# Kernel tuning notes

Measured on AMD Instinct MI355X. Metric: run time of the kernel, lower is better.

Reference implementation:

```python
import jax, jax.numpy as jnp
import numpy as np

B, T, I, H, C, S, V = 32, 64, 300, 168, 168, 512, 50257


def setup_inputs() -> dict:
    key = jax.random.key(0)
    ks = jax.random.split(key, 10)
    s = 0.05
    return {
        "x": jax.random.normal(ks[0], (B, T, I), jnp.float32),
        "context": jax.random.normal(ks[1], (B, S, C), jnp.float32),
        "context_lengths": jax.random.randint(ks[2], (B,), 1, S + 1),
        "W_ih": jax.random.normal(ks[3], (4 * H, I + C), jnp.float32) * s,
        "W_hh": jax.random.normal(ks[4], (4 * H, H), jnp.float32) * s,
        "b_ih": jnp.zeros((4 * H,), jnp.float32),
        "b_hh": jnp.zeros((4 * H,), jnp.float32),
        "att_Wx": jax.random.normal(ks[5], (H, H), jnp.float32) * s,
        "att_Ws": jax.random.normal(ks[6], (C, H), jnp.float32) * s,
        "att_b": jnp.zeros((H,), jnp.float32),
        "att_v": jax.random.normal(ks[7], (H,), jnp.float32) * s,
        "W_dec": jax.random.normal(ks[8], (V, H), jnp.float32) * s,
    }


def reference(x, context, context_lengths, W_ih, W_hh, b_ih, b_hh,
              att_Wx, att_Ws, att_b, att_v, W_dec):
    # x: (B, T, I); context: (B, S, C)
    b, t, _ = x.shape
    s_len = context.shape[1]
    h_dim = W_hh.shape[1]
    dtype = x.dtype

    # valid-position mask for attention over source context
    mask = jnp.arange(s_len)[None, :] < context_lengths[:, None]  # (B, S)
    # seq projection is time-invariant: precompute once outside the step loop
    seq_proj = jnp.einsum('bsc,ca->bsa', context, att_Ws)  # (B, S, H)

    h0 = jnp.zeros((b, h_dim), dtype)
    c0 = jnp.zeros((b, h_dim), dtype)

    def step(carry, x_t):
        h, c = carry
        # MLP (additive) attention: v . tanh(Wx h + Ws seq + b)
        e = jnp.einsum('bsa,a->bs',
                       jnp.tanh((h @ att_Wx)[:, None, :] + seq_proj + att_b),
                       att_v)  # (B, S)
        e = jnp.where(mask, e, jnp.asarray(-1e9, dtype))
        w = jax.nn.softmax(e, axis=-1)
        attn_ctx = jnp.einsum('bs,bsc->bc', w, context)  # (B, C)

        # concat input with attended context, single-layer LSTM cell
        rnn_in = jnp.concatenate([x_t, attn_ctx], axis=1)  # (B, I+C)
        gates = rnn_in @ W_ih.T + b_ih + h @ W_hh.T + b_hh  # (B, 4H)
        i_g, f_g, g_g, o_g = jnp.split(gates, 4, axis=1)    # torch ifgo order
        c_new = jax.nn.sigmoid(f_g) * c + jax.nn.sigmoid(i_g) * jnp.tanh(g_g)
        h_new = jax.nn.sigmoid(o_g) * jnp.tanh(c_new)

        dec = h_new @ W_dec.T  # (B, V), bias-free decode
        return (h_new, c_new), dec

    _, decs = jax.lax.scan(step, (h0, c0), jnp.swapaxes(x, 0, 1))  # (T, B, V)
    return jnp.swapaxes(decs, 0, 1)  # (B, T, V)
```

## Files before the change

kernel.cpp:

```cpp
#include <hip/hip_runtime.h>
#include <stdint.h>

#define BB 32
#define TT 64
#define ID 300
#define HH 168
#define SS 512
#define VV 50257
#define G4 672
#define IC 468
#define KP 192
#define NP 50304
#define NJ 8
#define RPB 21
#define CPB 84
#define KK 336
#define WKP 88
#define EPAD 170
#define SBLK 64

typedef float f32x4 __attribute__((ext_vector_type(4)));
typedef short bf16x8 __attribute__((ext_vector_type(8)));

__device__ __forceinline__ float bf2f(unsigned short u) {
  union { unsigned int i; float f; } v; v.i = ((unsigned int)u) << 16; return v.f;
}
__device__ __forceinline__ unsigned short f2bf(float f) {
  union { float f; unsigned int u; } v; v.f = f;
  unsigned int r = v.u + 0x7fffu + ((v.u >> 16) & 1u);
  return (unsigned short)(r >> 16);
}
__device__ __forceinline__ float rcpf(float x) { return __builtin_amdgcn_rcpf(x); }

__global__ void k_tr(const float* __restrict__ Wih, float* __restrict__ WihxT) {
  int idx = blockIdx.x * 256 + threadIdx.x;
  if (idx < ID * G4) {
    int k = idx / G4, i = idx - k * G4;
    WihxT[idx] = Wih[(size_t)i * IC + k];
  }
}

__global__ void k_seqproj(const float* __restrict__ ctx, const float* __restrict__ Ws,
                          unsigned short* __restrict__ ETs, unsigned short* __restrict__ ctxb) {
  const int b = blockIdx.x;
  const int s0 = blockIdx.y * 16;
  const int tid = threadIdx.x;
  __shared__ float ctxL[16 * HH];
  for (int idx = tid; idx < 16 * HH; idx += 256) {
    float v = ctx[(size_t)(b * SS + s0) * HH + idx];
    ctxL[idx] = v;
    ctxb[(size_t)(b * SS + s0) * HH + idx] = f2bf(v);
  }
  __syncthreads();
  #pragma unroll
  for (int o = 0; o < 11; ++o) {
    int idx = o * 256 + tid;
    if (idx < 16 * HH) {
      int s = idx / HH, h = idx - s * HH;
      const float* cr = &ctxL[s * HH];
      float acc = 0.f;
      #pragma unroll 4
      for (int c = 0; c < HH; ++c) acc = fmaf(cr[c], Ws[c * HH + h], acc);
      ETs[(size_t)(b * SS + s0 + s) * HH + h] = f2bf(__expf(2.f * acc));
    }
  }
}

__global__ void k_xproj(const float* __restrict__ x, const float* __restrict__ WihxT,
                        const float* __restrict__ bih, const float* __restrict__ bhh,
                        float* __restrict__ Xp) {
  const int t0 = blockIdx.x * 8;
  const int b = blockIdx.y;
  const int tid = threadIdx.x;
  __shared__ float xL[8 * ID];
  for (int idx = tid; idx < 8 * ID; idx += 256)
    xL[idx] = x[(size_t)(b * TT + t0) * ID + idx];
  __syncthreads();
  for (int i = tid; i < G4; i += 256) {
    float bias = bih[i] + bhh[i];
    float acc[8];
    #pragma unroll
    for (int tt = 0; tt < 8; ++tt) acc[tt] = bias;
    for (int k = 0; k < ID; ++k) {
      float w = WihxT[k * G4 + i];
      #pragma unroll
      for (int tt = 0; tt < 8; ++tt) acc[tt] += xL[tt * ID + k] * w;
    }
    #pragma unroll
    for (int tt = 0; tt < 8; ++tt)
      Xp[(size_t)(b * TT + t0 + tt) * G4 + i] = acc[tt];
  }
}

__global__ void k_wdec(const float* __restrict__ Wd, unsigned short* __restrict__ Wdb) {
  size_t idx = (size_t)blockIdx.x * 256 + threadIdx.x;
  int v = (int)(idx / KP), k = (int)(idx - (size_t)v * KP);
  float val = (v < VV && k < HH) ? Wd[(size_t)v * HH + k] : 0.f;
  Wdb[idx] = f2bf(val);
}

__global__ void k_prep(const float* __restrict__ Wih, const float* __restrict__ Whh,
                       const float* __restrict__ attWx, float* __restrict__ WgT,
                       unsigned short* __restrict__ WxS, unsigned int* __restrict__ flags,
                       unsigned short* __restrict__ hall) {
  int idx = blockIdx.x * 256 + threadIdx.x;
  const int T1 = NJ * KK * WKP;
  const int T2 = T1 + NJ * RPB * HH;
  const int T3 = T2 + 2 * BB * NJ * 64;
  const int T4 = T3 + BB * TT * (KP - HH);
  if (idx < T1) {
    int j = idx / (KK * WKP); int r = idx - j * KK * WKP;
    int k = r / WKP, col = r - k * WKP;
    float w = 0.f;
    if (col < CPB) {
      int gt = col / RPB, rr = col - gt * RPB;
      int gcol = gt * HH + j * RPB + rr;
      w = (k < HH) ? Wih[(size_t)gcol * IC + ID + k] : Whh[(size_t)gcol * HH + (k - HH)];
    }
    WgT[idx] = w;
  } else if (idx < T2) {
    int r = idx - T1;
    WxS[r] = f2bf(attWx[r]);
  } else if (idx < T3) {
    flags[idx - T2] = 0u;
  } else if (idx < T4) {
    int r = idx - T3;
    int bt = r / (KP - HH), c = r - bt * (KP - HH);
    hall[(size_t)bt * KP + HH + c] = 0;
  }
}

__global__ __launch_bounds__(512, 1) void k_recur(
    const int* __restrict__ lens, const float* __restrict__ attb,
    const float* __restrict__ attv, const float* __restrict__ WgT,
    const unsigned short* __restrict__ WxS, const unsigned short* __restrict__ ETs,
    const unsigned short* __restrict__ ctxb, const float* __restrict__ Xp,
    float* __restrict__ Hbuf, float* __restrict__ Pbuf, float* __restrict__ APbuf,
    unsigned int* __restrict__ flags, unsigned short* __restrict__ hall) {
  const int b = blockIdx.x & 31;
  const int j = blockIdx.x >> 5;
  const int tid = threadIdx.x;

  __shared__ float WgL[KK][WKP];
  __shared__ unsigned short EL[SBLK][EPAD];
  __shared__ unsigned short WxL[RPB][HH];
  __shared__ float scratch[512];
  __shared__ float redH[504], redC[504];
  __shared__ float gE[HH], hsh[HH], abL[HH], vL[HH], attn[HH];
  __shared__ float esh[SBLK], gatesL[CPB], hLoc[RPB], cLoc[RPB];
  __shared__ float denr_s, sumv_s, bsum_s;

  {
    const f32x4* src = (const f32x4*)(WgT + (size_t)j * KK * WKP);
    f32x4* dst = (f32x4*)WgL;
    for (int i = tid; i < KK * WKP / 4; i += 512) dst[i] = src[i];
  }
  for (int i = tid; i < SBLK * HH; i += 512) {
    int s = i / HH, h = i - s * HH;
    EL[s][h] = ETs[((size_t)b * SS + j * SBLK + s) * HH + h];
  }
  for (int i = tid; i < RPB * HH; i += 512)
    ((unsigned short*)WxL)[i] = WxS[(size_t)j * RPB * HH + i];
  if (tid < HH) { abL[tid] = attb[tid]; vL[tid] = attv[tid]; }
  if (tid < RPB) cLoc[tid] = 0.f;
  __syncthreads();
  if (tid == 0) {
    float s = 0.f;
    for (int h = 0; h < HH; ++h) s += vL[h];
    sumv_s = s;
  }
  const int len = lens[b];
  const int sbase = j * SBLK;
  unsigned int* fB = flags + (size_t)(b * NJ) * 64;
  unsigned int* fA = flags + (size_t)BB * NJ * 64 + (size_t)(b * NJ) * 64;
  __syncthreads();

  for (int t = 0; t < TT; ++t) {
    if (t > 0) {
      if (tid < NJ) {
        int g = 0;
        while (__hip_atomic_load(&fB[tid * 64], __ATOMIC_RELAXED,
                                 __HIP_MEMORY_SCOPE_AGENT) < (unsigned)t) {
          __builtin_amdgcn_s_sleep(2);
          if (++g > (1 << 27)) break;
        }
      }
      asm volatile("" ::: "memory");
      __syncthreads();
      if (tid < HH) {
        float a = abL[tid];
        #pragma unroll
        for (int jj = 0; jj < NJ; ++jj)
          a += __hip_atomic_load(&APbuf[((size_t)b * NJ + jj) * HH + tid],
                                 __ATOMIC_RELAXED, __HIP_MEMORY_SCOPE_AGENT);
        gE[tid] = __expf(2.f * a);
        hsh[tid] = __hip_atomic_load(&Hbuf[(size_t)b * HH + tid],
                                     __ATOMIC_RELAXED, __HIP_MEMORY_SCOPE_AGENT);
      }
    } else {
      if (tid < HH) { gE[tid] = __expf(2.f * abL[tid]); hsh[tid] = 0.f; }
    }
    __syncthreads();
    {
      int sl = tid & 63, hs = tid >> 6;
      const unsigned short* er = &EL[sl][hs * RPB];
      const int hb = hs * RPB;
      float ep = 0.f;
      #pragma unroll 7
      for (int i = 0; i < RPB; ++i)
        ep += vL[hb + i] * rcpf(fmaf(gE[hb + i], bf2f(er[i]), 1.f));
      scratch[hs * 64 + sl] = ep;
    }
    __syncthreads();
    if (tid < SBLK) {
      float tot = 0.f;
      #pragma unroll
      for (int hs = 0; hs < 8; ++hs) tot += scratch[hs * 64 + tid];
      float eh = (sbase + tid < len) ? __expf(sumv_s - 2.f * tot) : 0.f;
      esh[tid] = eh;
      float r = eh;
      #pragma unroll
      for (int off = 32; off; off >>= 1) r += __shfl_down(r, off);
      if (tid == 0) bsum_s = r;
    }
    __syncthreads();
    if (tid < 504) {
      int c = tid % HH, ch = tid / HH;
      const unsigned short* cb = ctxb + ((size_t)b * SS + sbase) * HH + c;
      float p = 0.f;
      for (int s = ch; s < SBLK; s += 3)
        p = fmaf(esh[s], bf2f(cb[(size_t)s * HH]), p);
      scratch[ch * HH + c] = p;
    }
    __syncthreads();
    if (tid < HH) {
      float p = scratch[tid] + scratch[HH + tid] + scratch[2 * HH + tid];
      __hip_atomic_store(&Pbuf[((size_t)b * NJ + j) * 176 + tid], p,
                         __ATOMIC_RELAXED, __HIP_MEMORY_SCOPE_AGENT);
    } else if (tid == HH) {
      __hip_atomic_store(&Pbuf[((size_t)b * NJ + j) * 176 + HH], bsum_s,
                         __ATOMIC_RELAXED, __HIP_MEMORY_SCOPE_AGENT);
    }
    __syncthreads();
    if (tid == 0) {
      asm volatile("s_waitcnt vmcnt(0)" ::: "memory");
      __hip_atomic_store(&fA[j * 64], (unsigned)(t + 1),
                         __ATOMIC_RELAXED, __HIP_MEMORY_SCOPE_AGENT);
    }
    if (tid < 504) {
      int col = tid % CPB, kc = tid / CPB;
      int k0 = HH + kc * 28;
      float acc = 0.f;
      #pragma unroll 7
      for (int i = 0; i < 28; ++i)
        acc = fmaf(WgL[k0 + i][col], hsh[kc * 28 + i], acc);
      redH[kc * CPB + col] = acc;
    }
    if (tid < NJ) {
      int g = 0;
      while (__hip_atomic_load(&fA[tid * 64], __ATOMIC_RELAXED,
                               __HIP_MEMORY_SCOPE_AGENT) < (unsigned)(t + 1)) {
        __builtin_amdgcn_s_sleep(2);
        if (++g > (1 << 27)) break;
      }
    }
    asm volatile("" ::: "memory");
    __syncthreads();
    if (tid < HH + 1) {
      float s = 0.f;
      #pragma unroll
      for (int jj = 0; jj < NJ; ++jj)
        s += __hip_atomic_load(&Pbuf[((size_t)b * NJ + jj) * 176 + tid],
                               __ATOMIC_RELAXED, __HIP_MEMORY_SCOPE_AGENT);
      if (tid < HH) scratch[tid] = s;
      else denr_s = 1.f / s;
    }
    __syncthreads();
    if (tid < HH) attn[tid] = scratch[tid] * denr_s;
    __syncthreads();
    if (tid < 504) {
      int col = tid % CPB, kc = tid / CPB;
      int k0 = kc * 28;
      float acc = 0.f;
      #pragma unroll 7
      for (int i = 0; i < 28; ++i)
        acc = fmaf(WgL[k0 + i][col], attn[k0 + i], acc);
      redC[kc * CPB + col] = acc;
    }
    __syncthreads();
    if (tid < CPB) {
      int gt = tid / RPB, rr = tid - gt * RPB;
      int gcol = gt * HH + j * RPB + rr;
      float g = Xp[((size_t)b * TT + t) * G4 + gcol];
      #pragma unroll
      for (int kc = 0; kc < 6; ++kc) g += redH[kc * CPB + tid] + redC[kc * CPB + tid];
      gatesL[tid] = g;
    }
    __syncthreads();
    if (tid < RPB) {
      float ig = gatesL[tid], fg = gatesL[RPB + tid];
      float gg = gatesL[2 * RPB + tid], og = gatesL[3 * RPB + tid];
      float si = rcpf(1.f + __expf(-ig));
      float sf = rcpf(1.f + __expf(-fg));
      float so = rcpf(1.f + __expf(-og));
      float tg = 1.f - 2.f * rcpf(1.f + __expf(2.f * gg));
      float cn = fmaf(sf, cLoc[tid], si * tg);
      float tc = 1.f - 2.f * rcpf(1.f + __expf(2.f * cn));
      float hn = so * tc;
      cLoc[tid] = cn; hLoc[tid] = hn;
      hall[((size_t)b * TT + t) * KP + j * RPB + tid] = f2bf(hn);
      __hip_atomic_store(&Hbuf[(size_t)b * HH + j * RPB + tid], hn,
                         __ATOMIC_RELAXED, __HIP_MEMORY_SCOPE_AGENT);
    }
    __syncthreads();
    if (tid < 504) {
      int col = tid % HH, ch = tid / HH;
      float acc = 0.f;
      #pragma unroll
      for (int r = ch * 7; r < ch * 7 + 7; ++r)
        acc = fmaf(hLoc[r], bf2f(WxL[r][col]), acc);
      scratch[ch * HH + col] = acc;
    }
    __syncthreads();
    if (tid < HH) {
      float a = scratch[tid] + scratch[HH + tid] + scratch[2 * HH + tid];
      __hip_atomic_store(&APbuf[((size_t)b * NJ + j) * HH + tid], a,
                         __ATOMIC_RELAXED, __HIP_MEMORY_SCOPE_AGENT);
    }
    __syncthreads();
    if (tid == 0) {
      asm volatile("s_waitcnt vmcnt(0)" ::: "memory");
      __hip_atomic_store(&fB[j * 64], (unsigned)(t + 1),
                         __ATOMIC_RELAXED, __HIP_MEMORY_SCOPE_AGENT);
    }
  }
}

__global__ __launch_bounds__(256) void k_decode(const unsigned short* __restrict__ hallb,
                                                const unsigned short* __restrict__ wdb,
                                                float* __restrict__ out) {
  __shared__ __align__(16) unsigned short As[128 * 64];
  __shared__ __align__(16) unsigned short Bs[128 * 64];
  const int tid = threadIdx.x;
  const int n0 = blockIdx.x * 128, m0 = blockIdx.y * 128;
  const int lane = tid & 63, wid = tid >> 6;
  const int wm = wid >> 1, wn = wid & 1;
  const int lr = lane & 15, lk = lane >> 4;
  f32x4 acc[4][4];
  #pragma unroll
  for (int i = 0; i < 4; ++i)
    #pragma unroll
    for (int jj = 0; jj < 4; ++jj) acc[i][jj] = (f32x4)0.f;

  for (int k0 = 0; k0 < KP; k0 += 64) {
    if (k0) __syncthreads();
    #pragma unroll
    for (int i = 0; i < 4; ++i) {
      int flat = i * 256 + tid;
      int row = flat >> 3;
      int col = (flat & 7) * 8;
      uint4 va = *(const uint4*)(hallb + (size_t)(m0 + row) * KP + k0 + col);
      *(uint4*)&As[row * 64 + col] = va;
      uint4 vb = *(const uint4*)(wdb + (size_t)(n0 + row) * KP + k0 + col);
      *(uint4*)&Bs[row * 64 + col] = vb;
    }
    __syncthreads();
    #pragma unroll
    for (int kk = 0; kk < 64; kk += 32) {
      bf16x8 af[4], bfr[4];
      #pragma unroll
      for (int mi = 0; mi < 4; ++mi)
        af[mi] = *(const bf16x8*)&As[(wm * 64 + mi * 16 + lr) * 64 + kk + lk * 8];
      #pragma unroll
      for (int ni = 0; ni < 4; ++ni)
        bfr[ni] = *(const bf16x8*)&Bs[(wn * 64 + ni * 16 + lr) * 64 + kk + lk * 8];
      #pragma unroll
      for (int mi = 0; mi < 4; ++mi)
        #pragma unroll
        for (int ni = 0; ni < 4; ++ni)
          acc[mi][ni] = __builtin_amdgcn_mfma_f32_16x16x32_bf16(
              af[mi], bfr[ni], acc[mi][ni], 0, 0, 0);
    }
  }
  #pragma unroll
  for (int mi = 0; mi < 4; ++mi)
    #pragma unroll
    for (int ni = 0; ni < 4; ++ni) {
      int col = n0 + wn * 64 + ni * 16 + lr;
      if (col < VV) {
        #pragma unroll
        for (int r = 0; r < 4; ++r) {
          int row = m0 + wm * 64 + mi * 16 + lk * 4 + r;
          out[(size_t)row * VV + col] = acc[mi][ni][r];
        }
      }
    }
}

extern "C" void kernel_launch(void* const* d_in, const int* in_sizes, int n_in,
                              void* d_out, int out_size, void* d_ws, size_t ws_size,
                              hipStream_t stream) {
  (void)in_sizes; (void)n_in; (void)out_size; (void)ws_size;
  const float* x     = (const float*)d_in[0];
  const float* ctx   = (const float*)d_in[1];
  const int*   lens  = (const int*)d_in[2];
  const float* Wih   = (const float*)d_in[3];
  const float* Whh   = (const float*)d_in[4];
  const float* bih   = (const float*)d_in[5];
  const float* bhh   = (const float*)d_in[6];
  const float* attWx = (const float*)d_in[7];
  const float* attWs = (const float*)d_in[8];
  const float* attb  = (const float*)d_in[9];
  const float* attv  = (const float*)d_in[10];
  const float* Wdec  = (const float*)d_in[11];
  float* out = (float*)d_out;

  char* base = (char*)d_ws;
  size_t off = 0;
  auto alloc = [&](size_t bytes) -> void* {
    off = (off + 255) & ~(size_t)255;
    void* p = base + off;
    off += bytes;
    return p;
  };
  unsigned short* ETs  = (unsigned short*)alloc((size_t)BB * SS * HH * 2);
  unsigned short* ctxb = (unsigned short*)alloc((size_t)BB * SS * HH * 2);
  float*          Xp   = (float*)alloc((size_t)BB * TT * G4 * 4);
  float*          WihxT= (float*)alloc((size_t)ID * G4 * 4);
  unsigned short* hall = (unsigned short*)alloc((size_t)BB * TT * KP * 2);
  unsigned short* Wdb  = (unsigned short*)alloc((size_t)NP * KP * 2);
  float*          WgT  = (float*)alloc((size_t)NJ * KK * WKP * 4);
  unsigned short* WxS  = (unsigned short*)alloc((size_t)NJ * RPB * HH * 2);
  float*          Hbuf = (float*)alloc((size_t)BB * HH * 4);
  float*          Pbuf = (float*)alloc((size_t)BB * NJ * 176 * 4);
  float*          APbuf= (float*)alloc((size_t)BB * NJ * HH * 4);
  unsigned int*   flags= (unsigned int*)alloc((size_t)2 * BB * NJ * 64 * 4);

  k_tr<<<dim3((ID * G4 + 255) / 256), dim3(256), 0, stream>>>(Wih, WihxT);
  k_seqproj<<<dim3(BB, SS / 16), dim3(256), 0, stream>>>(ctx, attWs, ETs, ctxb);
  k_xproj<<<dim3(TT / 8, BB), dim3(256), 0, stream>>>(x, WihxT, bih, bhh, Xp);
  k_wdec<<<dim3((int)(((size_t)NP * KP) / 256)), dim3(256), 0, stream>>>(Wdec, Wdb);
  {
    const int TOT = NJ * KK * WKP + NJ * RPB * HH + 2 * BB * NJ * 64 + BB * TT * (KP - HH);
    k_prep<<<dim3((TOT + 255) / 256), dim3(256), 0, stream>>>(Wih, Whh, attWx, WgT,
                                                              WxS, flags, hall);
  }
  {
    const int* a0 = lens; const float* a1 = attb; const float* a2 = attv;
    const float* a3 = WgT; const unsigned short* a4 = WxS;
    const unsigned short* a5 = ETs; const unsigned short* a6 = ctxb;
    const float* a7 = Xp; float* a8 = Hbuf; float* a9 = Pbuf; float* a10 = APbuf;
    unsigned int* a11 = flags; unsigned short* a12 = hall;
    void* args[] = { &a0, &a1, &a2, &a3, &a4, &a5, &a6, &a7, &a8, &a9, &a10, &a11, &a12 };
    hipLaunchCooperativeKernel((void*)k_recur, dim3(BB * NJ), dim3(512), args, 0, stream);
  }
  k_decode<<<dim3(NP / 128, (BB * TT) / 128), dim3(256), 0, stream>>>(hall, Wdb, out);
}
```

Measured before the change: 919.8 us.

## Merge prep kernels, trim recurrence barriers, enlarge decode GEMM tiles

Several unrelated changes land together. Five preprocessing launches become two: a single prep kernel that also vectorizes the W_dec bf16 conversion, and a combined seq-projection/x-projection kernel. The recurrent step loses several __syncthreads by doing the score reduction with wave shuffles, summing the softmax denominator inside the Pbuf gather, and prefetching Xp gates into registers. The decode GEMM moves to 256x256 tiles with 512 threads and padded LDS rows to cut bank conflicts, at the cost of more registers and fewer blocks.

```diff
diff --git a/kernel.cpp b/kernel.cpp
--- a/kernel.cpp
+++ b/kernel.cpp
@@ -10,7 +10,7 @@
 #define G4 672
 #define IC 468
 #define KP 192
-#define NP 50304
+#define NP2 50432
 #define NJ 8
 #define RPB 21
 #define CPB 84
@@ -18,6 +18,7 @@
 #define WKP 88
 #define EPAD 170
 #define SBLK 64
+#define LP 72
 
 typedef float f32x4 __attribute__((ext_vector_type(4)));
 typedef short bf16x8 __attribute__((ext_vector_type(8)));
@@ -32,84 +33,44 @@
 }
 __device__ __forceinline__ float rcpf(float x) { return __builtin_amdgcn_rcpf(x); }
 
-__global__ void k_tr(const float* __restrict__ Wih, float* __restrict__ WihxT) {
-  int idx = blockIdx.x * 256 + threadIdx.x;
-  if (idx < ID * G4) {
-    int k = idx / G4, i = idx - k * G4;
-    WihxT[idx] = Wih[(size_t)i * IC + k];
-  }
-}
-
-__global__ void k_seqproj(const float* __restrict__ ctx, const float* __restrict__ Ws,
-                          unsigned short* __restrict__ ETs, unsigned short* __restrict__ ctxb) {
-  const int b = blockIdx.x;
-  const int s0 = blockIdx.y * 16;
-  const int tid = threadIdx.x;
-  __shared__ float ctxL[16 * HH];
-  for (int idx = tid; idx < 16 * HH; idx += 256) {
-    float v = ctx[(size_t)(b * SS + s0) * HH + idx];
-    ctxL[idx] = v;
-    ctxb[(size_t)(b * SS + s0) * HH + idx] = f2bf(v);
-  }
-  __syncthreads();
-  #pragma unroll
-  for (int o = 0; o < 11; ++o) {
-    int idx = o * 256 + tid;
-    if (idx < 16 * HH) {
-      int s = idx / HH, h = idx - s * HH;
-      const float* cr = &ctxL[s * HH];
-      float acc = 0.f;
-      #pragma unroll 4
-      for (int c = 0; c < HH; ++c) acc = fmaf(cr[c], Ws[c * HH + h], acc);
-      ETs[(size_t)(b * SS + s0 + s) * HH + h] = f2bf(__expf(2.f * acc));
-    }
-  }
-}
-
-__global__ void k_xproj(const float* __restrict__ x, const float* __restrict__ WihxT,
-                        const float* __restrict__ bih, const float* __restrict__ bhh,
-                        float* __restrict__ Xp) {
-  const int t0 = blockIdx.x * 8;
-  const int b = blockIdx.y;
-  const int tid = threadIdx.x;
-  __shared__ float xL[8 * ID];
-  for (int idx = tid; idx < 8 * ID; idx += 256)
-    xL[idx] = x[(size_t)(b * TT + t0) * ID + idx];
-  __syncthreads();
-  for (int i = tid; i < G4; i += 256) {
-    float bias = bih[i] + bhh[i];
-    float acc[8];
-    #pragma unroll
-    for (int tt = 0; tt < 8; ++tt) acc[tt] = bias;
-    for (int k = 0; k < ID; ++k) {
-      float w = WihxT[k * G4 + i];
-      #pragma unroll
-      for (int tt = 0; tt < 8; ++tt) acc[tt] += xL[tt * ID + k] * w;
-    }
-    #pragma unroll
-    for (int tt = 0; tt < 8; ++tt)
-      Xp[(size_t)(b * TT + t0 + tt) * G4 + i] = acc[tt];
-  }
-}
-
-__global__ void k_wdec(const float* __restrict__ Wd, unsigned short* __restrict__ Wdb) {
-  size_t idx = (size_t)blockIdx.x * 256 + threadIdx.x;
-  int v = (int)(idx / KP), k = (int)(idx - (size_t)v * KP);
-  float val = (v < VV && k < HH) ? Wd[(size_t)v * HH + k] : 0.f;
-  Wdb[idx] = f2bf(val);
-}
-
-__global__ void k_prep(const float* __restrict__ Wih, const float* __restrict__ Whh,
-                       const float* __restrict__ attWx, float* __restrict__ WgT,
-                       unsigned short* __restrict__ WxS, unsigned int* __restrict__ flags,
-                       unsigned short* __restrict__ hall) {
-  int idx = blockIdx.x * 256 + threadIdx.x;
+#define NB_WDEC 4728
+#define NB_TR   788
+__global__ void k_prepall(const float* __restrict__ Wih, const float* __restrict__ Whh,
+                          const float* __restrict__ attWx, const float* __restrict__ Wd,
+                          float* __restrict__ WihxT, unsigned short* __restrict__ Wdb,
+                          float* __restrict__ WgT, unsigned short* __restrict__ WxS,
+                          unsigned int* __restrict__ flags, unsigned short* __restrict__ hall) {
+  const int bid = blockIdx.x, tid = threadIdx.x;
+  if (bid < NB_WDEC) {
+    size_t e0 = ((size_t)bid * 256 + tid) * 8;
+    int v = (int)(e0 / KP), k = (int)(e0 - (size_t)v * KP);
+    unsigned short o[8];
+    if (v < VV && k < HH) {
+      const float* src = Wd + (size_t)v * HH + k;
+      #pragma unroll
+      for (int i = 0; i < 8; ++i) o[i] = f2bf(src[i]);
+    } else {
+      #pragma unroll
+      for (int i = 0; i < 8; ++i) o[i] = 0;
+    }
+    *(uint4*)(Wdb + e0) = *(const uint4*)o;
+    return;
+  }
+  if (bid < NB_WDEC + NB_TR) {
+    int idx = (bid - NB_WDEC) * 256 + tid;
+    if (idx < ID * G4) {
+      int k = idx / G4, i = idx - k * G4;
+      WihxT[idx] = Wih[(size_t)i * IC + k];
+    }
+    return;
+  }
+  int idx = (bid - NB_WDEC - NB_TR) * 256 + tid;
   const int T1 = NJ * KK * WKP;
   const int T2 = T1 + NJ * RPB * HH;
   const int T3 = T2 + 2 * BB * NJ * 64;
   const int T4 = T3 + BB * TT * (KP - HH);
   if (idx < T1) {
-    int j = idx / (KK * WKP); int r = idx - j * KK * WKP;
+    int j = idx / (KK * WKP); int r = idx - j * (KK * WKP);
     int k = r / WKP, col = r - k * WKP;
     float w = 0.f;
     if (col < CPB) {
@@ -130,6 +91,58 @@
   }
 }
 
+__global__ void k_seqxp(const float* __restrict__ ctx, const float* __restrict__ Ws,
+                        const float* __restrict__ x, const float* __restrict__ WihxT,
+                        const float* __restrict__ bih, const float* __restrict__ bhh,
+                        unsigned short* __restrict__ ETs, unsigned short* __restrict__ ctxb,
+                        float* __restrict__ Xp) {
+  __shared__ float sbuf[2688];
+  const int tid = threadIdx.x;
+  if (blockIdx.x < 1024) {
+    const int b = blockIdx.x & 31;
+    const int s0 = (blockIdx.x >> 5) * 16;
+    for (int idx = tid; idx < 16 * HH; idx += 256) {
+      float v = ctx[(size_t)(b * SS + s0) * HH + idx];
+      sbuf[idx] = v;
+      ctxb[(size_t)(b * SS + s0) * HH + idx] = f2bf(v);
+    }
+    __syncthreads();
+    #pragma unroll
+    for (int o = 0; o < 11; ++o) {
+      int idx = o * 256 + tid;
+      if (idx < 16 * HH) {
+        int s = idx / HH, h = idx - s * HH;
+        const float* cr = &sbuf[s * HH];
+        float acc = 0.f;
+        #pragma unroll 4
+        for (int c = 0; c < HH; ++c) acc = fmaf(cr[c], Ws[c * HH + h], acc);
+        ETs[(size_t)(b * SS + s0 + s) * HH + h] = f2bf(__expf(2.f * acc));
+      }
+    }
+  } else {
+    const int r = blockIdx.x - 1024;
+    const int t0 = (r & 7) * 8;
+    const int b = r >> 3;
+    for (int idx = tid; idx < 8 * ID; idx += 256)
+      sbuf[idx] = x[(size_t)(b * TT + t0) * ID + idx];
+    __syncthreads();
+    for (int i = tid; i < G4; i += 256) {
+      float bias = bih[i] + bhh[i];
+      float acc[8];
+      #pragma unroll
+      for (int tt = 0; tt < 8; ++tt) acc[tt] = bias;
+      for (int k = 0; k < ID; ++k) {
+        float w = WihxT[k * G4 + i];
+        #pragma unroll
+        for (int tt = 0; tt < 8; ++tt) acc[tt] += sbuf[tt * ID + k] * w;
+      }
+      #pragma unroll
+      for (int tt = 0; tt < 8; ++tt)
+        Xp[(size_t)(b * TT + t0 + tt) * G4 + i] = acc[tt];
+    }
+  }
+}
+
 __global__ __launch_bounds__(512, 1) void k_recur(
     const int* __restrict__ lens, const float* __restrict__ attb,
     const float* __restrict__ attv, const float* __restrict__ WgT,
@@ -147,8 +160,8 @@
   __shared__ float scratch[512];
   __shared__ float redH[504], redC[504];
   __shared__ float gE[HH], hsh[HH], abL[HH], vL[HH], attn[HH];
-  __shared__ float esh[SBLK], gatesL[CPB], hLoc[RPB], cLoc[RPB];
-  __shared__ float denr_s, sumv_s, bsum_s;
+  __shared__ float esh[SBLK], hLoc[RPB], cLoc[RPB], wsum[8];
+  __shared__ float sumv_s, bsum_s;
 
   {
     const f32x4* src = (const f32x4*)(WgT + (size_t)j * KK * WKP);
@@ -176,6 +189,11 @@
   __syncthreads();
 
   for (int t = 0; t < TT; ++t) {
+    float xpr0 = 0.f, xpr1 = 0.f, xpr2 = 0.f, xpr3 = 0.f;
+    if (tid < RPB) {
+      const float* xp = Xp + ((size_t)b * TT + t) * G4 + j * RPB + tid;
+      xpr0 = xp[0]; xpr1 = xp[HH]; xpr2 = xp[2 * HH]; xpr3 = xp[3 * HH];
+    }
     if (t > 0) {
       if (tid < NJ) {
         int g = 0;
@@ -187,41 +205,38 @@
       }
       asm volatile("" ::: "memory");
       __syncthreads();
-      if (tid < HH) {
-        float a = abL[tid];
+    }
+    if (tid < HH) {
+      float a = abL[tid];
+      if (t > 0) {
         #pragma unroll
         for (int jj = 0; jj < NJ; ++jj)
           a += __hip_atomic_load(&APbuf[((size_t)b * NJ + jj) * HH + tid],
                                  __ATOMIC_RELAXED, __HIP_MEMORY_SCOPE_AGENT);
-        gE[tid] = __expf(2.f * a);
         hsh[tid] = __hip_atomic_load(&Hbuf[(size_t)b * HH + tid],
                                      __ATOMIC_RELAXED, __HIP_MEMORY_SCOPE_AGENT);
-      }
-    } else {
-      if (tid < HH) { gE[tid] = __expf(2.f * abL[tid]); hsh[tid] = 0.f; }
+      } else {
+        hsh[tid] = 0.f;
+      }
+      gE[tid] = __expf(2.f * a);
     }
     __syncthreads();
     {
-      int sl = tid & 63, hs = tid >> 6;
-      const unsigned short* er = &EL[sl][hs * RPB];
-      const int hb = hs * RPB;
+      int w = tid >> 6, lane = tid & 63;
+      int sl = w * 8 + (lane >> 3);
+      int hg = lane & 7;
+      const unsigned short* er = &EL[sl][hg * RPB];
+      const int hb = hg * RPB;
       float ep = 0.f;
       #pragma unroll 7
       for (int i = 0; i < RPB; ++i)
         ep += vL[hb + i] * rcpf(fmaf(gE[hb + i], bf2f(er[i]), 1.f));
-      scratch[hs * 64 + sl] = ep;
-    }
-    __syncthreads();
-    if (tid < SBLK) {
-      float tot = 0.f;
-      #pragma unroll
-      for (int hs = 0; hs < 8; ++hs) tot += scratch[hs * 64 + tid];
-      float eh = (sbase + tid < len) ? __expf(sumv_s - 2.f * tot) : 0.f;
-      esh[tid] = eh;
-      float r = eh;
-      #pragma unroll
-      for (int off = 32; off; off >>= 1) r += __shfl_down(r, off);
-      if (tid == 0) bsum_s = r;
+      ep += __shfl_xor(ep, 1); ep += __shfl_xor(ep, 2); ep += __shfl_xor(ep, 4);
+      float eh = (sbase + sl < len) ? __expf(sumv_s - 2.f * ep) : 0.f;
+      float ws = (hg == 0) ? eh : 0.f;
+      ws += __shfl_xor(ws, 8); ws += __shfl_xor(ws, 16); ws += __shfl_xor(ws, 32);
+      if (lane == 0) wsum[w] = ws;
+      if (hg == 0) esh[sl] = eh;
     }
     __syncthreads();
     if (tid < 504) {
@@ -231,6 +246,11 @@
       for (int s = ch; s < SBLK; s += 3)
         p = fmaf(esh[s], bf2f(cb[(size_t)s * HH]), p);
       scratch[ch * HH + c] = p;
+    } else if (tid == 504) {
+      float bs = 0.f;
+      #pragma unroll
+      for (int w = 0; w < 8; ++w) bs += wsum[w];
+      bsum_s = bs;
     }
     __syncthreads();
     if (tid < HH) {
@@ -266,17 +286,16 @@
     }
     asm volatile("" ::: "memory");
     __syncthreads();
-    if (tid < HH + 1) {
-      float s = 0.f;
-      #pragma unroll
-      for (int jj = 0; jj < NJ; ++jj)
-        s += __hip_atomic_load(&Pbuf[((size_t)b * NJ + jj) * 176 + tid],
-                               __ATOMIC_RELAXED, __HIP_MEMORY_SCOPE_AGENT);
-      if (tid < HH) scratch[tid] = s;
-      else denr_s = 1.f / s;
-    }
-    __syncthreads();
-    if (tid < HH) attn[tid] = scratch[tid] * denr_s;
+    if (tid < HH) {
+      float s = 0.f, den = 0.f;
+      #pragma unroll
+      for (int jj = 0; jj < NJ; ++jj) {
+        const float* pb = &Pbuf[((size_t)b * NJ + jj) * 176];
+        s += __hip_atomic_load(&pb[tid], __ATOMIC_RELAXED, __HIP_MEMORY_SCOPE_AGENT);
+        den += __hip_atomic_load(&pb[HH], __ATOMIC_RELAXED, __HIP_MEMORY_SCOPE_AGENT);
+      }
+      attn[tid] = s * rcpf(den);
+    }
     __syncthreads();
     if (tid < 504) {
       int col = tid % CPB, kc = tid / CPB;
@@ -288,22 +307,21 @@
       redC[kc * CPB + col] = acc;
     }
     __syncthreads();
-    if (tid < CPB) {
-      int gt = tid / RPB, rr = tid - gt * RPB;
-      int gcol = gt * HH + j * RPB + rr;
-      float g = Xp[((size_t)b * TT + t) * G4 + gcol];
-      #pragma unroll
-      for (int kc = 0; kc < 6; ++kc) g += redH[kc * CPB + tid] + redC[kc * CPB + tid];
-      gatesL[tid] = g;
-    }
-    __syncthreads();
     if (tid < RPB) {
-      float ig = gatesL[tid], fg = gatesL[RPB + tid];
-      float gg = gatesL[2 * RPB + tid], og = gatesL[3 * RPB + tid];
-      float si = rcpf(1.f + __expf(-ig));
-      float sf = rcpf(1.f + __expf(-fg));
-      float so = rcpf(1.f + __expf(-og));
-      float tg = 1.f - 2.f * rcpf(1.f + __expf(2.f * gg));
+      float g0 = xpr0, g1 = xpr1, g2 = xpr2, g3 = xpr3;
+      #pragma unroll
+      for (int kc = 0; kc < 6; ++kc) {
+        const float* rh = &redH[kc * CPB];
+        const float* rc = &redC[kc * CPB];
+        g0 += rh[tid] + rc[tid];
+        g1 += rh[RPB + tid] + rc[RPB + tid];
+        g2 += rh[2 * RPB + tid] + rc[2 * RPB + tid];
+        g3 += rh[3 * RPB + tid] + rc[3 * RPB + tid];
+      }
+      float si = rcpf(1.f + __expf(-g0));
+      float sf = rcpf(1.f + __expf(-g1));
+      float tg = 1.f - 2.f * rcpf(1.f + __expf(2.f * g2));
+      float so = rcpf(1.f + __expf(-g3));
       float cn = fmaf(sf, cLoc[tid], si * tg);
       float tc = 1.f - 2.f * rcpf(1.f + __expf(2.f * cn));
       float hn = so * tc;
@@ -336,19 +354,19 @@
   }
 }
 
-__global__ __launch_bounds__(256) void k_decode(const unsigned short* __restrict__ hallb,
-                                                const unsigned short* __restrict__ wdb,
-                                                float* __restrict__ out) {
-  __shared__ __align__(16) unsigned short As[128 * 64];
-  __shared__ __align__(16) unsigned short Bs[128 * 64];
+__global__ __launch_bounds__(512, 1) void k_decode(const unsigned short* __restrict__ hallb,
+                                                   const unsigned short* __restrict__ wdb,
+                                                   float* __restrict__ out) {
+  __shared__ __align__(16) unsigned short As[256 * LP];
+  __shared__ __align__(16) unsigned short Bs[256 * LP];
   const int tid = threadIdx.x;
-  const int n0 = blockIdx.x * 128, m0 = blockIdx.y * 128;
+  const int n0 = blockIdx.x * 256, m0 = blockIdx.y * 256;
   const int lane = tid & 63, wid = tid >> 6;
-  const int wm = wid >> 1, wn = wid & 1;
+  const int wm = wid >> 2, wn = wid & 3;
   const int lr = lane & 15, lk = lane >> 4;
-  f32x4 acc[4][4];
+  f32x4 acc[8][4];
   #pragma unroll
-  for (int i = 0; i < 4; ++i)
+  for (int i = 0; i < 8; ++i)
     #pragma unroll
     for (int jj = 0; jj < 4; ++jj) acc[i][jj] = (f32x4)0.f;
 
@@ -356,26 +374,26 @@
     if (k0) __syncthreads();
     #pragma unroll
     for (int i = 0; i < 4; ++i) {
-      int flat = i * 256 + tid;
+      int flat = i * 512 + tid;
       int row = flat >> 3;
-      int col = (flat & 7) * 8;
-      uint4 va = *(const uint4*)(hallb + (size_t)(m0 + row) * KP + k0 + col);
-      *(uint4*)&As[row * 64 + col] = va;
-      uint4 vb = *(const uint4*)(wdb + (size_t)(n0 + row) * KP + k0 + col);
-      *(uint4*)&Bs[row * 64 + col] = vb;
+      int c8 = flat & 7;
+      uint4 va = *(const uint4*)(hallb + (size_t)(m0 + row) * KP + k0 + c8 * 8);
+      *(uint4*)&As[row * LP + c8 * 8] = va;
+      uint4 vb = *(const uint4*)(wdb + (size_t)(n0 + row) * KP + k0 + c8 * 8);
+      *(uint4*)&Bs[row * LP + c8 * 8] = vb;
     }
     __syncthreads();
     #pragma unroll
     for (int kk = 0; kk < 64; kk += 32) {
-      bf16x8 af[4], bfr[4];
-      #pragma unroll
-      for (int mi = 0; mi < 4; ++mi)
-        af[mi] = *(const bf16x8*)&As[(wm * 64 + mi * 16 + lr) * 64 + kk + lk * 8];
+      bf16x8 af[8], bfr[4];
+      #pragma unroll
+      for (int mi = 0; mi < 8; ++mi)
+        af[mi] = *(const bf16x8*)&As[(wm * 128 + mi * 16 + lr) * LP + kk + lk * 8];
       #pragma unroll
       for (int ni = 0; ni < 4; ++ni)
-        bfr[ni] = *(const bf16x8*)&Bs[(wn * 64 + ni * 16 + lr) * 64 + kk + lk * 8];
-      #pragma unroll
-      for (int mi = 0; mi < 4; ++mi)
+        bfr[ni] = *(const bf16x8*)&Bs[(wn * 64 + ni * 16 + lr) * LP + kk + lk * 8];
+      #pragma unroll
+      for (int mi = 0; mi < 8; ++mi)
         #pragma unroll
         for (int ni = 0; ni < 4; ++ni)
           acc[mi][ni] = __builtin_amdgcn_mfma_f32_16x16x32_bf16(
@@ -383,14 +401,14 @@
     }
   }
   #pragma unroll
-  for (int mi = 0; mi < 4; ++mi)
+  for (int mi = 0; mi < 8; ++mi)
     #pragma unroll
     for (int ni = 0; ni < 4; ++ni) {
       int col = n0 + wn * 64 + ni * 16 + lr;
       if (col < VV) {
         #pragma unroll
         for (int r = 0; r < 4; ++r) {
-          int row = m0 + wm * 64 + mi * 16 + lk * 4 + r;
+          int row = m0 + wm * 128 + mi * 16 + lk * 4 + r;
           out[(size_t)row * VV + col] = acc[mi][ni][r];
         }
       }
@@ -428,7 +446,7 @@
   float*          Xp   = (float*)alloc((size_t)BB * TT * G4 * 4);
   float*          WihxT= (float*)alloc((size_t)ID * G4 * 4);
   unsigned short* hall = (unsigned short*)alloc((size_t)BB * TT * KP * 2);
-  unsigned short* Wdb  = (unsigned short*)alloc((size_t)NP * KP * 2);
+  unsigned short* Wdb  = (unsigned short*)alloc((size_t)NP2 * KP * 2);
   float*          WgT  = (float*)alloc((size_t)NJ * KK * WKP * 4);
   unsigned short* WxS  = (unsigned short*)alloc((size_t)NJ * RPB * HH * 2);
   float*          Hbuf = (float*)alloc((size_t)BB * HH * 4);
@@ -436,15 +454,14 @@
   float*          APbuf= (float*)alloc((size_t)BB * NJ * HH * 4);
   unsigned int*   flags= (unsigned int*)alloc((size_t)2 * BB * NJ * 64 * 4);
 
-  k_tr<<<dim3((ID * G4 + 255) / 256), dim3(256), 0, stream>>>(Wih, WihxT);
-  k_seqproj<<<dim3(BB, SS / 16), dim3(256), 0, stream>>>(ctx, attWs, ETs, ctxb);
-  k_xproj<<<dim3(TT / 8, BB), dim3(256), 0, stream>>>(x, WihxT, bih, bhh, Xp);
-  k_wdec<<<dim3((int)(((size_t)NP * KP) / 256)), dim3(256), 0, stream>>>(Wdec, Wdb);
   {
-    const int TOT = NJ * KK * WKP + NJ * RPB * HH + 2 * BB * NJ * 64 + BB * TT * (KP - HH);
-    k_prep<<<dim3((TOT + 255) / 256), dim3(256), 0, stream>>>(Wih, Whh, attWx, WgT,
-                                                              WxS, flags, hall);
-  }
+    const int TOTP = NJ * KK * WKP + NJ * RPB * HH + 2 * BB * NJ * 64 + BB * TT * (KP - HH);
+    const int NBP = (TOTP + 255) / 256;
+    k_prepall<<<dim3(NB_WDEC + NB_TR + NBP), dim3(256), 0, stream>>>(
+        Wih, Whh, attWx, Wdec, WihxT, Wdb, WgT, WxS, flags, hall);
+  }
+  k_seqxp<<<dim3(1024 + 256), dim3(256), 0, stream>>>(ctx, attWs, x, WihxT,
+                                                      bih, bhh, ETs, ctxb, Xp);
   {
     const int* a0 = lens; const float* a1 = attb; const float* a2 = attv;
     const float* a3 = WgT; const unsigned short* a4 = WxS;
@@ -454,5 +471,5 @@
     void* args[] = { &a0, &a1, &a2, &a3, &a4, &a5, &a6, &a7, &a8, &a9, &a10, &a11, &a12 };
     hipLaunchCooperativeKernel((void*)k_recur, dim3(BB * NJ), dim3(512), args, 0, stream);
   }
-  k_decode<<<dim3(NP / 128, (BB * TT) / 128), dim3(256), 0, stream>>>(hall, Wdb, out);
-}
+  k_decode<<<dim3(NP2 / 256, (BB * TT) / 256), dim3(512), 0, stream>>>(hall, Wdb, out);
+}
```

New measurement: 814.1 us. -11.5%, faster.
